# Optimization experiments

Measured on AMD Instinct MI355X. Metric: run time of the kernel, lower is better.

The kernel has to match this reference:

```python
import jax, jax.numpy as jnp
import numpy as np

B, T, V, E, M, L = 1024, 64, 1024, 512, 1024, 32
PE, PO = M // 2, (M - 1) // 2  # even/odd pair counts


def complex_normalize(x, eps=1e-8):
    mag = jnp.sqrt((x.real ** 2 + x.imag ** 2).sum(-1, keepdims=True) + eps)
    return x / mag


def pair_unitary(v0, v1, t, p, r):
    # 2x2 MZI unitary applied to pairs (v0, v1); t/p/r are (P,) broadcast over batch
    c, s = jnp.cos(t), jnp.sin(t)
    eip, eir = jnp.exp(1j * p), jnp.exp(1j * r)
    u11 = eip * c * eir
    u12 = eip * (1j * s)
    u21 = (1j * s) * eir
    u22 = c
    return u11 * v0 + u12 * v1, u21 * v0 + u22 * v1


def setup_inputs() -> dict:
    key = jax.random.key(0)
    ks = jax.random.split(key, 16)
    sE = 1.0 / np.sqrt(E)
    return {
        "context_tokens": jax.random.randint(ks[0], (B, T), 0, V),
        "embed": 0.02 * jax.random.normal(ks[1], (V, E), jnp.float32),
        "W_ih": sE * jax.random.normal(ks[2], (3 * E, E), jnp.float32),
        "W_hh": sE * jax.random.normal(ks[3], (3 * E, E), jnp.float32),
        "b_ih": jnp.zeros((3 * E,), jnp.float32),
        "b_hh": jnp.zeros((3 * E,), jnp.float32),
        "Wc": 0.02 * jax.random.normal(ks[4], (2 * M, E), jnp.float32),
        "bc": jnp.zeros((2 * M,), jnp.float32),
        "phase": 0.1 * jax.random.normal(ks[5], (L, M), jnp.float32),
        "theta_e": 0.1 * jax.random.normal(ks[6], (L, PE), jnp.float32),
        "phi_e": 0.1 * jax.random.normal(ks[7], (L, PE), jnp.float32),
        "rho_e": 0.1 * jax.random.normal(ks[8], (L, PE), jnp.float32),
        "theta_o": 0.1 * jax.random.normal(ks[9], (L, PO), jnp.float32),
        "phi_o": 0.1 * jax.random.normal(ks[10], (L, PO), jnp.float32),
        "rho_o": 0.1 * jax.random.normal(ks[11], (L, PO), jnp.float32),
        "R_real": 0.01 * jax.random.normal(ks[12], (V, M), jnp.float32),
        "R_imag": 0.01 * jax.random.normal(ks[13], (V, M), jnp.float32),
    }


def reference(context_tokens, embed, W_ih, W_hh, b_ih, b_hh, Wc, bc,
              phase, theta_e, phi_e, rho_e, theta_o, phi_o, rho_o,
              R_real, R_imag):
    # --- ContextEncoder: embedding + GRU (torch gate order r,z,n) ---
    x = embed[context_tokens]                      # (B,T,E)
    x_gates = x @ W_ih.T + b_ih                    # (B,T,3E) precomputed input gates

    def gru_step(h, xg):
        ir, iz, in_ = jnp.split(xg, 3, axis=-1)
        hr, hz, hn = jnp.split(h @ W_hh.T + b_hh, 3, axis=-1)
        r = jax.nn.sigmoid(ir + hr)
        z = jax.nn.sigmoid(iz + hz)
        n = jnp.tanh(in_ + r * hn)
        return (1.0 - z) * n + z * h, None

    h0 = jnp.zeros((x.shape[0], embed.shape[1]), x.dtype)
    h, _ = jax.lax.scan(gru_step, h0, jnp.swapaxes(x_gates, 0, 1))  # (B,E)

    zc = h @ Wc.T + bc                              # (B,2M)
    re, im = jnp.split(zc, 2, axis=-1)
    psi = complex_normalize(re + 1j * im)           # (B,M) complex64

    # --- QuantumCore: stack of MZI layers ---
    def layer(psi, p):
        ph, te, pe, re_, to, po, ro = p
        psi = psi * jnp.exp(1j * ph)
        D = psi.shape[1]
        # even pairs (0,1),(2,3),...
        v0, v1 = pair_unitary(psi[:, 0::2], psi[:, 1::2], te, pe, re_)
        psi = psi.at[:, 0::2].set(v0).at[:, 1::2].set(v1)
        # odd pairs (1,2),(3,4),...
        v0, v1 = pair_unitary(psi[:, 1:D - 1:2], psi[:, 2:D:2], to, po, ro)
        psi = psi.at[:, 1:D - 1:2].set(v0).at[:, 2:D:2].set(v1)
        return complex_normalize(psi), None

    psi, _ = jax.lax.scan(layer, psi, (phase, theta_e, phi_e, rho_e,
                                       theta_o, phi_o, rho_o))

    # --- QuantumReadout: Born rule log-probs ---
    R = R_real + 1j * R_imag                        # (V,M)
    amps = psi @ R.T                                # (B,V) complex
    log_mag_sq = jnp.log(amps.real ** 2 + amps.imag ** 2 + 1e-12)
    return log_mag_sq - jax.scipy.special.logsumexp(log_mag_sq, axis=-1, keepdims=True)
```

## Files before the change

### kernel.cpp

```cpp
#include <hip/hip_runtime.h>
#include <math.h>

typedef __bf16 bf16_t;
typedef bf16_t bf16x8 __attribute__((ext_vector_type(8)));
typedef float  f32x4  __attribute__((ext_vector_type(4)));

#define B_  1024
#define T_  64
#define V_  1024
#define E_  512
#define M_  1024
#define L_  32
#define PE_ 512
#define PO_ 511
#define G3_ 1536
#define M2_ 2048

#define MFMA_BF16 __builtin_amdgcn_mfma_f32_16x16x32_bf16

__device__ __forceinline__ void stage16f(float* lds_base, const float* gsrc) {
  __builtin_amdgcn_global_load_lds(
      (const __attribute__((address_space(1))) unsigned int*)gsrc,
      (__attribute__((address_space(3))) unsigned int*)lds_base, 16, 0, 0);
}
__device__ __forceinline__ void stage16b(bf16_t* lds_base, const bf16_t* gsrc) {
  __builtin_amdgcn_global_load_lds(
      (const __attribute__((address_space(1))) unsigned int*)gsrc,
      (__attribute__((address_space(3))) unsigned int*)lds_base, 16, 0, 0);
}

__device__ __forceinline__ size_t tiled_off(int row, int k) {
  return ((size_t)(row >> 4) * 16 + (k >> 5)) * 512 +
         (size_t)(((k >> 3) & 3) * 16 + (row & 15)) * 8 + (k & 7);
}

__device__ __forceinline__ void split_chunk(const float* __restrict__ src,
                                            bf16_t* __restrict__ hi,
                                            bf16_t* __restrict__ lo, int blk,
                                            int tid) {
  int i4 = (blk * 256 + tid) * 4;
  float4 v = *(const float4*)&src[i4];
  float vv[4] = {v.x, v.y, v.z, v.w};
#pragma unroll
  for (int j = 0; j < 4; j++) {
    bf16_t h = (bf16_t)vv[j];
    hi[i4 + j] = h;
    lo[i4 + j] = (bf16_t)(vv[j] - (float)h);
  }
}

__global__ __launch_bounds__(256) void prep_all(
    const float* __restrict__ embed, bf16_t* __restrict__ emb_hi,
    bf16_t* __restrict__ emb_lo, const float* __restrict__ W_ih,
    bf16_t* __restrict__ wih_hi, bf16_t* __restrict__ wih_lo,
    const float* __restrict__ Wc, bf16_t* __restrict__ wc_hi,
    bf16_t* __restrict__ wc_lo, const float* __restrict__ R_real,
    bf16_t* __restrict__ rr_hi, bf16_t* __restrict__ rr_lo,
    const float* __restrict__ R_imag, bf16_t* __restrict__ ri_hi,
    bf16_t* __restrict__ ri_lo, const float* __restrict__ W_hh,
    bf16_t* __restrict__ Wp_hi, bf16_t* __restrict__ Wp_lo,
    const float* __restrict__ phase, const float* __restrict__ th_e,
    const float* __restrict__ ph_e, const float* __restrict__ rh_e,
    float* __restrict__ Uep, const float* __restrict__ th_o,
    const float* __restrict__ ph_o, const float* __restrict__ rh_o,
    float* __restrict__ Uop) {
  const int bid = blockIdx.x, tid = threadIdx.x;
  if (bid < 512) {
    split_chunk(embed, emb_hi, emb_lo, bid, tid);
  } else if (bid < 1280) {
    split_chunk(W_ih, wih_hi, wih_lo, bid - 512, tid);
  } else if (bid < 2304) {
    split_chunk(Wc, wc_hi, wc_lo, bid - 1280, tid);
  } else if (bid < 3328) {
    split_chunk(R_real, rr_hi, rr_lo, bid - 2304, tid);
  } else if (bid < 4352) {
    split_chunk(R_imag, ri_hi, ri_lo, bid - 3328, tid);
  } else if (bid < 5888) {
    int q = bid - 4352;
    int c = q / 96, loc = q % 96;
    int g = loc >> 5, el = loc & 31;
    const float* src = &W_hh[(size_t)(g * 512 + c * 32 + el) * 512];
    if (tid < 64) {
      int k0 = tid * 8;
      float4 v0 = *(const float4*)&src[k0];
      float4 v1 = *(const float4*)&src[k0 + 4];
      float vv[8] = {v0.x, v0.y, v0.z, v0.w, v1.x, v1.y, v1.z, v1.w};
      bf16x8 h8, l8;
#pragma unroll
      for (int j = 0; j < 8; j++) {
        bf16_t h = (bf16_t)vv[j];
        h8[j] = h;
        l8[j] = (bf16_t)(vv[j] - (float)h);
      }
      size_t toff = tiled_off(q, k0);
      *(bf16x8*)&Wp_hi[toff] = h8;
      *(bf16x8*)&Wp_lo[toff] = l8;
    }
  } else if (bid < 5952) {
    int idx = (bid - 5888) * 256 + tid;
    if (idx < L_ * PE_) {
      int l = idx >> 9, p = idx & 511;
      float t = th_e[idx], pp = ph_e[idx], r = rh_e[idx];
      float c = cosf(t), s = sinf(t);
      float cp = cosf(pp), sp = sinf(pp), cr = cosf(r), sr = sinf(r);
      float u11r = c * (cp * cr - sp * sr), u11i = c * (cp * sr + sp * cr);
      float u12r = -s * sp, u12i = s * cp;
      float u21r = -s * sr, u21i = s * cr;
      float u22r = c, u22i = 0.0f;
      float f0 = phase[l * M_ + 2 * p], f1 = phase[l * M_ + 2 * p + 1];
      float c0 = cosf(f0), s0 = sinf(f0), c1 = cosf(f1), s1 = sinf(f1);
      float a, b;
      a = u11r * c0 - u11i * s0; b = u11r * s0 + u11i * c0; u11r = a; u11i = b;
      a = u21r * c0 - u21i * s0; b = u21r * s0 + u21i * c0; u21r = a; u21i = b;
      a = u12r * c1 - u12i * s1; b = u12r * s1 + u12i * c1; u12r = a; u12i = b;
      a = u22r * c1 - u22i * s1; b = u22r * s1 + u22i * c1; u22r = a; u22i = b;
      int j = p & 3, ln = (p >> 2) & 63, hh = p >> 8;
      size_t base = (size_t)l * 4096 + (size_t)(j * 4 + hh) * 256 + ln * 4;
      *(float4*)&Uep[base]       = make_float4(u11r, u11i, u12r, u12i);
      *(float4*)&Uep[base + 512] = make_float4(u21r, u21i, u22r, u22i);
    }
  } else {
    int idx = (bid - 5952) * 256 + tid;
    if (idx < L_ * PO_) {
      int l = idx / PO_, p = idx % PO_;
      float t = th_o[idx], pp = ph_o[idx], r = rh_o[idx];
      float c = cosf(t), s = sinf(t);
      float cp = cosf(pp), sp = sinf(pp), cr = cosf(r), sr = sinf(r);
      int j = p & 3, ln = (p >> 2) & 63, hh = p >> 8;
      size_t base = (size_t)l * 4096 + (size_t)(j * 4 + hh) * 256 + ln * 4;
      *(float4*)&Uop[base] = make_float4(c * (cp * cr - sp * sr),
                                         c * (cp * sr + sp * cr), -s * sp,
                                         s * cp);
      *(float4*)&Uop[base + 512] = make_float4(-s * sr, s * cr, c, 0.0f);
    }
  }
}

__global__ __launch_bounds__(256) void gemm_bt_mfma_split(
    const bf16_t* __restrict__ Ah, const bf16_t* __restrict__ Al,
    const bf16_t* __restrict__ Bh, const bf16_t* __restrict__ Bl,
    float* __restrict__ C, int Ndim, int K) {
  __shared__ bf16_t sAh[64 * 32], sAl[64 * 32], sBh[64 * 32], sBl[64 * 32];
  const int tid = threadIdx.x;
  const int m0 = blockIdx.y * 64, n0 = blockIdx.x * 64;
  const int wave = tid >> 6, lane = tid & 63;
  const int wr = wave >> 1, wc = wave & 1;
  const int quad = lane >> 4, l16 = lane & 15;
  f32x4 acc[2][2] = {};
  const int srow = tid >> 2, sk = (tid & 3) * 8;

  for (int k0 = 0; k0 < K; k0 += 32) {
    bf16x8 ah = *(const bf16x8*)&Ah[(size_t)(m0 + srow) * K + k0 + sk];
    bf16x8 al = *(const bf16x8*)&Al[(size_t)(m0 + srow) * K + k0 + sk];
    bf16x8 bh = *(const bf16x8*)&Bh[(size_t)(n0 + srow) * K + k0 + sk];
    bf16x8 bl = *(const bf16x8*)&Bl[(size_t)(n0 + srow) * K + k0 + sk];
    __syncthreads();
    *(bf16x8*)&sAh[srow * 32 + sk] = ah;
    *(bf16x8*)&sAl[srow * 32 + sk] = al;
    *(bf16x8*)&sBh[srow * 32 + sk] = bh;
    *(bf16x8*)&sBl[srow * 32 + sk] = bl;
    __syncthreads();
    bf16x8 fAh[2], fAl[2], fBh[2], fBl[2];
#pragma unroll
    for (int i = 0; i < 2; i++) {
      fAh[i] = *(const bf16x8*)&sAh[(wr * 32 + i * 16 + l16) * 32 + quad * 8];
      fAl[i] = *(const bf16x8*)&sAl[(wr * 32 + i * 16 + l16) * 32 + quad * 8];
      fBh[i] = *(const bf16x8*)&sBh[(wc * 32 + i * 16 + l16) * 32 + quad * 8];
      fBl[i] = *(const bf16x8*)&sBl[(wc * 32 + i * 16 + l16) * 32 + quad * 8];
    }
#pragma unroll
    for (int i = 0; i < 2; i++)
#pragma unroll
      for (int j = 0; j < 2; j++) {
        acc[i][j] = MFMA_BF16(fAh[i], fBh[j], acc[i][j], 0, 0, 0);
        acc[i][j] = MFMA_BF16(fAh[i], fBl[j], acc[i][j], 0, 0, 0);
        acc[i][j] = MFMA_BF16(fAl[i], fBh[j], acc[i][j], 0, 0, 0);
      }
  }
#pragma unroll
  for (int i = 0; i < 2; i++)
#pragma unroll
    for (int j = 0; j < 2; j++)
#pragma unroll
      for (int r = 0; r < 4; r++) {
        int row = wr * 32 + i * 16 + quad * 4 + r;
        int col = wc * 32 + j * 16 + l16;
        C[(size_t)(m0 + row) * Ndim + n0 + col] = acc[i][j][r];
      }
}

__global__ __launch_bounds__(512) void gru_step11(
    const bf16_t* __restrict__ Hh, const bf16_t* __restrict__ Hl,
    const bf16_t* __restrict__ Wph, const bf16_t* __restrict__ Wpl,
    const int* __restrict__ tok, const float* __restrict__ eg,
    const float* __restrict__ b_ih, const float* __restrict__ b_hh,
    bf16_t* __restrict__ Oh, bf16_t* __restrict__ Ol, int t, int final_) {
  __shared__ bf16_t sB[2][2][24 * 512];
  __shared__ float sC[2][64 * 100];
  __shared__ float sbih[96], sbhh[96];
  const int tid = threadIdx.x;
  const int g = tid >> 8;
  const int gtid = tid & 255;
  const int ct = blockIdx.y, m0 = blockIdx.x * 64;
  const int n0e = ct * 32;
  const int wg = gtid >> 6, lane = tid & 63;
  const int wr = wg >> 1, wc = wg & 1;
  const int quad = lane >> 4, l16 = lane & 15;

#define STAGE_B(buf, it)                                                      \
  {                                                                           \
    _Pragma("unroll") for (int r = 0; r < 6; r++) {                           \
      int c = wg * 6 + r;                                                     \
      int f = (c >= 12) ? (c - 12) : c;                                       \
      int j = f >> 1, ks = f & 1;                                             \
      const bf16_t* srcp = (c < 12) ? Wph : Wpl;                              \
      stage16b(&sB[buf][g][c * 512],                                          \
               &srcp[(size_t)(ct * 6 + j) * 8192 +                            \
                     (size_t)(g * 8 + (it) * 2 + ks) * 512 + lane * 8]);      \
    }                                                                         \
  }

  STAGE_B(0, 0);

  if (tid < 96) {
    sbih[tid] = b_ih[(tid >> 5) * 512 + n0e + (tid & 31)];
    sbhh[tid] = b_hh[(tid >> 5) * 512 + n0e + (tid & 31)];
  }

  float pir[4], piz[4], pin[4], phv[4];
#pragma unroll
  for (int u = 0; u < 4; u++) {
    int flat = u * 512 + tid;
    int row = flat >> 5, el = flat & 31;
    int bb = m0 + row, eG = n0e + el;
    int tk = tok[bb * T_ + t];
    pir[u] = eg[(size_t)tk * G3_ + eG];
    piz[u] = eg[(size_t)tk * G3_ + 512 + eG];
    pin[u] = eg[(size_t)tk * G3_ + 1024 + eG];
    size_t toff = tiled_off(bb, eG);
    phv[u] = (float)Hh[toff] + (float)Hl[toff];
  }

  const size_t aB0 = (size_t)((m0 >> 4) + wr * 2 + 0) * 8192 + (size_t)g * 4096 + lane * 8;
  const size_t aB1 = (size_t)((m0 >> 4) + wr * 2 + 1) * 8192 + (size_t)g * 4096 + lane * 8;

  f32x4 acc[2][3] = {};
  __syncthreads();
#pragma unroll
  for (int it = 0; it < 4; ++it) {
    const int buf = it & 1;
    if (it < 3) STAGE_B(buf ^ 1, it + 1);
    const bf16_t* sBg = &sB[buf][g][0];
#pragma unroll
    for (int ks2 = 0; ks2 < 2; ++ks2) {
      const int kb = it * 2 + ks2;
      const int ko = kb * 512;
      bf16x8 fah[2], fal[2], fbh[3], fbl[3];
      fah[0] = *(const bf16x8*)&Hh[aB0 + ko];
      fah[1] = *(const bf16x8*)&Hh[aB1 + ko];
      fal[0] = *(const bf16x8*)&Hl[aB0 + ko];
      fal[1] = *(const bf16x8*)&Hl[aB1 + ko];
#pragma unroll
      for (int j = 0; j < 3; j++) {
        int f = (wc * 3 + j) * 2 + ks2;
        fbh[j] = *(const bf16x8*)&sBg[f * 512 + lane * 8];
        fbl[j] = *(const bf16x8*)&sBg[(f + 12) * 512 + lane * 8];
      }
#pragma unroll
      for (int i = 0; i < 2; i++)
#pragma unroll
        for (int j = 0; j < 3; j++) {
          acc[i][j] = MFMA_BF16(fah[i], fbh[j], acc[i][j], 0, 0, 0);
          acc[i][j] = MFMA_BF16(fah[i], fbl[j], acc[i][j], 0, 0, 0);
          acc[i][j] = MFMA_BF16(fal[i], fbh[j], acc[i][j], 0, 0, 0);
        }
    }
    __syncthreads();
  }
#undef STAGE_B
#pragma unroll
  for (int i = 0; i < 2; i++)
#pragma unroll
    for (int j = 0; j < 3; j++)
#pragma unroll
      for (int r = 0; r < 4; r++)
        sC[g][(wr * 32 + i * 16 + quad * 4 + r) * 100 + wc * 48 + j * 16 + l16] =
            acc[i][j][r];
  __syncthreads();
#pragma unroll
  for (int u = 0; u < 4; u++) {
    int flat = u * 512 + tid;
    int row = flat >> 5, el = flat & 31;
    int bb = m0 + row, eG = n0e + el;
    float ir = pir[u] + sbih[el];
    float iz = piz[u] + sbih[32 + el];
    float in_ = pin[u] + sbih[64 + el];
    float hr = sC[0][row * 100 + el] + sC[1][row * 100 + el] + sbhh[el];
    float hz = sC[0][row * 100 + 32 + el] + sC[1][row * 100 + 32 + el] + sbhh[32 + el];
    float hn = sC[0][row * 100 + 64 + el] + sC[1][row * 100 + 64 + el] + sbhh[64 + el];
    float r = 1.0f / (1.0f + __expf(-(ir + hr)));
    float z = 1.0f / (1.0f + __expf(-(iz + hz)));
    float targ = fminf(fmaxf(in_ + r * hn, -15.0f), 15.0f);
    float e2 = __expf(2.0f * targ);
    float n = (e2 - 1.0f) / (e2 + 1.0f);
    float hnew = (1.0f - z) * n + z * phv[u];
    bf16_t hh = (bf16_t)hnew;
    bf16_t ll = (bf16_t)(hnew - (float)hh);
    if (final_) {
      size_t hidx = (size_t)bb * 512 + eG;
      Oh[hidx] = hh;
      Ol[hidx] = ll;
    } else {
      size_t toff = tiled_off(bb, eG);
      Oh[toff] = hh;
      Ol[toff] = ll;
    }
  }
}

__device__ inline void apply_u(float4 A, float4 Bv, float& x0r, float& x0i,
                               float& x1r, float& x1i) {
  float n0r = A.x * x0r - A.y * x0i + A.z * x1r - A.w * x1i;
  float n0i = A.x * x0i + A.y * x0r + A.z * x1i + A.w * x1r;
  float n1r = Bv.x * x0r - Bv.y * x0i + Bv.z * x1r - Bv.w * x1i;
  float n1i = Bv.x * x0i + Bv.y * x0r + Bv.z * x1i + Bv.w * x1r;
  x0r = n0r; x0i = n0i; x1r = n1r; x1i = n1i;
}

__global__ __launch_bounds__(256) void qc6(
    const float* __restrict__ zc, const float* __restrict__ bc,
    const float* __restrict__ Uep, const float* __restrict__ Uop,
    bf16_t* __restrict__ prh, bf16_t* __restrict__ prl,
    bf16_t* __restrict__ pih, bf16_t* __restrict__ pil) {
  __shared__ float sU[2][8192];
  __shared__ float sred[4];
  __shared__ float4 sEx[2][2][2];
  const int tid = threadIdx.x;
  const int wave = tid >> 6, lane = tid & 63;
  const int wb = wave >> 1, h = wave & 1;
  const int b = blockIdx.x * 2 + wb;
  const int e0 = h * 512 + lane * 8;

#define STAGE_L(l, buf)                                                       \
  {                                                                           \
    _Pragma("unroll") for (int r = 0; r < 8; r++) {                           \
      int c = wave * 8 + r;                                                   \
      const float* src = (c < 16)                                             \
          ? &Uep[(size_t)(l) * 4096 + c * 256 + lane * 4]                     \
          : &Uop[(size_t)(l) * 4096 + (c - 16) * 256 + lane * 4];             \
      stage16f(&sU[buf][c * 256], src);                                       \
    }                                                                         \
  }

  float xr[8], xi[8];
  {
    const float4* zr4 = (const float4*)&zc[(size_t)b * M2_ + e0];
    const float4* zi4 = (const float4*)&zc[(size_t)b * M2_ + M_ + e0];
    const float4* br4 = (const float4*)&bc[e0];
    const float4* bi4 = (const float4*)&bc[M_ + e0];
#pragma unroll
    for (int q = 0; q < 2; q++) {
      float4 a = zr4[q], bb = br4[q];
      xr[4 * q + 0] = a.x + bb.x; xr[4 * q + 1] = a.y + bb.y;
      xr[4 * q + 2] = a.z + bb.z; xr[4 * q + 3] = a.w + bb.w;
      float4 c2 = zi4[q], d = bi4[q];
      xi[4 * q + 0] = c2.x + d.x; xi[4 * q + 1] = c2.y + d.y;
      xi[4 * q + 2] = c2.z + d.z; xi[4 * q + 3] = c2.w + d.w;
    }
  }
  STAGE_L(0, 0);
  {
    float s = 0.0f;
#pragma unroll
    for (int k = 0; k < 8; k++) s += xr[k] * xr[k] + xi[k] * xi[k];
    for (int off = 32; off; off >>= 1) s += __shfl_xor(s, off);
    if (lane == 0) sred[wave] = s;
    __syncthreads();
    float inv = 1.0f / sqrtf(sred[2 * wb] + sred[2 * wb + 1] + 1e-8f);
#pragma unroll
    for (int k = 0; k < 8; k++) { xr[k] *= inv; xi[k] *= inv; }
  }
  if (h == 0 && lane == 63) sEx[0][wb][0] = make_float4(xr[6], xi[6], xr[7], xi[7]);
  if (h == 1 && lane == 0)  sEx[0][wb][1] = make_float4(xr[0], xi[0], xr[1], xi[1]);
  __syncthreads();

#pragma unroll 1
  for (int l = 0; l < L_; ++l) {
    const int buf = l & 1;
    if (l + 1 < L_) STAGE_L(l + 1, 1 - buf);
    const float* Ub = &sU[buf][0];
    const float* Ob = &sU[buf][4096];
    float4 par = make_float4(0.f, 0.f, 0.f, 0.f);
    if (h == 0 && lane == 63) par = sEx[buf][wb][1];
    if (h == 1 && lane == 0)  par = sEx[buf][wb][0];
#pragma unroll
    for (int j = 0; j < 4; j++) {
      float4 A  = *(const float4*)&Ub[(j * 4 + h) * 256 + lane * 4];
      float4 Bv = *(const float4*)&Ub[(j * 4 + 2 + h) * 256 + lane * 4];
      apply_u(A, Bv, xr[2 * j], xi[2 * j], xr[2 * j + 1], xi[2 * j + 1]);
    }
    float exr = 0.f, exi = 0.f;
    if (h == 0 && lane == 63) {
      float4 Ae = *(const float4*)&Ub[1 * 256];
      exr = Ae.x * par.x - Ae.y * par.y + Ae.z * par.z - Ae.w * par.w;
      exi = Ae.x * par.y + Ae.y * par.x + Ae.z * par.w + Ae.w * par.z;
    }
    if (h == 1 && lane == 0) {
      float4 Be = *(const float4*)&Ub[14 * 256 + 252];
      exr = Be.x * par.x - Be.y * par.y + Be.z * par.z - Be.w * par.w;
      exi = Be.x * par.y + Be.y * par.x + Be.z * par.w + Be.w * par.z;
    }
#pragma unroll
    for (int j = 0; j < 3; j++) {
      float4 A  = *(const float4*)&Ob[(j * 4 + h) * 256 + lane * 4];
      float4 Bv = *(const float4*)&Ob[(j * 4 + 2 + h) * 256 + lane * 4];
      apply_u(A, Bv, xr[2 * j + 1], xi[2 * j + 1], xr[2 * j + 2], xi[2 * j + 2]);
    }
    float nr = __shfl_down(xr[0], 1), ni = __shfl_down(xi[0], 1);
    if (h == 0 && lane == 63) { nr = exr; ni = exi; }
    float srr = 0.f, sii = 0.f;
    if (!(h == 1 && lane == 63)) {
      float4 A3 = *(const float4*)&Ob[(12 + h) * 256 + lane * 4];
      float4 B3 = *(const float4*)&Ob[(14 + h) * 256 + lane * 4];
      float n0r = A3.x * xr[7] - A3.y * xi[7] + A3.z * nr - A3.w * ni;
      float n0i = A3.x * xi[7] + A3.y * xr[7] + A3.z * ni + A3.w * nr;
      srr = B3.x * xr[7] - B3.y * xi[7] + B3.z * nr - B3.w * ni;
      sii = B3.x * xi[7] + B3.y * xr[7] + B3.z * ni + B3.w * nr;
      xr[7] = n0r; xi[7] = n0i;
    }
    float nx0r = 0.f, nx0i = 0.f;
    if (h == 1 && lane == 0) {
      float4 Bc = *(const float4*)&Ob[14 * 256 + 252];
      nx0r = Bc.x * exr - Bc.y * exi + Bc.z * xr[0] - Bc.w * xi[0];
      nx0i = Bc.x * exi + Bc.y * exr + Bc.z * xi[0] + Bc.w * xr[0];
    }
    float rr = __shfl_up(srr, 1), ri2 = __shfl_up(sii, 1);
    if (lane > 0) { xr[0] = rr; xi[0] = ri2; }
    if (h == 1 && lane == 0) { xr[0] = nx0r; xi[0] = nx0i; }
    if (h == 0 && lane == 63)
      sEx[1 - buf][wb][0] = make_float4(xr[6], xi[6], xr[7], xi[7]);
    if (h == 1 && lane == 0)
      sEx[1 - buf][wb][1] = make_float4(xr[0], xi[0], xr[1], xi[1]);
    __syncthreads();
  }
#undef STAGE_L
  size_t base = (size_t)b * M_ + e0;
  bf16x8 vh, vl, wh, wl;
#pragma unroll
  for (int k = 0; k < 8; k++) {
    float vr = xr[k], vi = xi[k];
    bf16_t h1 = (bf16_t)vr;
    vh[k] = h1; vl[k] = (bf16_t)(vr - (float)h1);
    bf16_t h2 = (bf16_t)vi;
    wh[k] = h2; wl[k] = (bf16_t)(vi - (float)h2);
  }
  *(bf16x8*)&prh[base] = vh;
  *(bf16x8*)&prl[base] = vl;
  *(bf16x8*)&pih[base] = wh;
  *(bf16x8*)&pil[base] = wl;
}

__global__ __launch_bounds__(256) void readout_mfma(
    const bf16_t* __restrict__ Arh, const bf16_t* __restrict__ Arl,
    const bf16_t* __restrict__ Aih, const bf16_t* __restrict__ Ail,
    const bf16_t* __restrict__ Brh, const bf16_t* __restrict__ Brl,
    const bf16_t* __restrict__ Bih, const bf16_t* __restrict__ Bil,
    float* __restrict__ out) {
  __shared__ bf16_t sArh[64 * 32], sArl[64 * 32], sAih[64 * 32], sAil[64 * 32];
  __shared__ bf16_t sBrh[64 * 32], sBrl[64 * 32], sBih[64 * 32], sBil[64 * 32];
  const int tid = threadIdx.x;
  const int b0 = blockIdx.y * 64, v0 = blockIdx.x * 64;
  const int wave = tid >> 6, lane = tid & 63;
  const int wr = wave >> 1, wc = wave & 1;
  const int quad = lane >> 4, l16 = lane & 15;
  f32x4 aP[2][2] = {}, aQ[2][2] = {}, aI[2][2] = {};
  const int srow = tid >> 2, sk = (tid & 3) * 8;

  for (int k0 = 0; k0 < M_; k0 += 32) {
    size_t aoff = (size_t)(b0 + srow) * M_ + k0 + sk;
    size_t boff = (size_t)(v0 + srow) * M_ + k0 + sk;
    bf16x8 v0r = *(const bf16x8*)&Arh[aoff];
    bf16x8 v1r = *(const bf16x8*)&Arl[aoff];
    bf16x8 v2r = *(const bf16x8*)&Aih[aoff];
    bf16x8 v3r = *(const bf16x8*)&Ail[aoff];
    bf16x8 v4r = *(const bf16x8*)&Brh[boff];
    bf16x8 v5r = *(const bf16x8*)&Brl[boff];
    bf16x8 v6r = *(const bf16x8*)&Bih[boff];
    bf16x8 v7r = *(const bf16x8*)&Bil[boff];
    __syncthreads();
    *(bf16x8*)&sArh[srow * 32 + sk] = v0r;
    *(bf16x8*)&sArl[srow * 32 + sk] = v1r;
    *(bf16x8*)&sAih[srow * 32 + sk] = v2r;
    *(bf16x8*)&sAil[srow * 32 + sk] = v3r;
    *(bf16x8*)&sBrh[srow * 32 + sk] = v4r;
    *(bf16x8*)&sBrl[srow * 32 + sk] = v5r;
    *(bf16x8*)&sBih[srow * 32 + sk] = v6r;
    *(bf16x8*)&sBil[srow * 32 + sk] = v7r;
    __syncthreads();
    bf16x8 fArh[2], fArl[2], fAih[2], fAil[2], fBrh[2], fBrl[2], fBih[2], fBil[2];
#pragma unroll
    for (int i = 0; i < 2; i++) {
      int ra = (wr * 32 + i * 16 + l16) * 32 + quad * 8;
      int rb = (wc * 32 + i * 16 + l16) * 32 + quad * 8;
      fArh[i] = *(const bf16x8*)&sArh[ra];
      fArl[i] = *(const bf16x8*)&sArl[ra];
      fAih[i] = *(const bf16x8*)&sAih[ra];
      fAil[i] = *(const bf16x8*)&sAil[ra];
      fBrh[i] = *(const bf16x8*)&sBrh[rb];
      fBrl[i] = *(const bf16x8*)&sBrl[rb];
      fBih[i] = *(const bf16x8*)&sBih[rb];
      fBil[i] = *(const bf16x8*)&sBil[rb];
    }
#pragma unroll
    for (int i = 0; i < 2; i++)
#pragma unroll
      for (int j = 0; j < 2; j++) {
        aP[i][j] = MFMA_BF16(fArh[i], fBrh[j], aP[i][j], 0, 0, 0);
        aP[i][j] = MFMA_BF16(fArh[i], fBrl[j], aP[i][j], 0, 0, 0);
        aP[i][j] = MFMA_BF16(fArl[i], fBrh[j], aP[i][j], 0, 0, 0);
        aQ[i][j] = MFMA_BF16(fAih[i], fBih[j], aQ[i][j], 0, 0, 0);
        aQ[i][j] = MFMA_BF16(fAih[i], fBil[j], aQ[i][j], 0, 0, 0);
        aQ[i][j] = MFMA_BF16(fAil[i], fBih[j], aQ[i][j], 0, 0, 0);
        aI[i][j] = MFMA_BF16(fArh[i], fBih[j], aI[i][j], 0, 0, 0);
        aI[i][j] = MFMA_BF16(fArh[i], fBil[j], aI[i][j], 0, 0, 0);
        aI[i][j] = MFMA_BF16(fArl[i], fBih[j], aI[i][j], 0, 0, 0);
        aI[i][j] = MFMA_BF16(fAih[i], fBrh[j], aI[i][j], 0, 0, 0);
        aI[i][j] = MFMA_BF16(fAih[i], fBrl[j], aI[i][j], 0, 0, 0);
        aI[i][j] = MFMA_BF16(fAil[i], fBrh[j], aI[i][j], 0, 0, 0);
      }
  }
#pragma unroll
  for (int i = 0; i < 2; i++)
#pragma unroll
    for (int j = 0; j < 2; j++)
#pragma unroll
      for (int r = 0; r < 4; r++) {
        int row = wr * 32 + i * 16 + quad * 4 + r;
        int col = wc * 32 + j * 16 + l16;
        float re = aP[i][j][r] - aQ[i][j][r];
        float im = aI[i][j][r];
        out[(size_t)(b0 + row) * V_ + v0 + col] = logf(re * re + im * im + 1e-12f);
      }
}

__global__ __launch_bounds__(256) void lse_kernel(float* __restrict__ out) {
  __shared__ float redm[4], reds[4];
  const int b = blockIdx.x, t = threadIdx.x;
  float4 v = *(float4*)&out[(size_t)b * V_ + 4 * t];
  float mx = fmaxf(fmaxf(v.x, v.y), fmaxf(v.z, v.w));
  for (int off = 32; off; off >>= 1) mx = fmaxf(mx, __shfl_down(mx, off, 64));
  if ((t & 63) == 0) redm[t >> 6] = mx;
  __syncthreads();
  mx = fmaxf(fmaxf(redm[0], redm[1]), fmaxf(redm[2], redm[3]));
  float s = expf(v.x - mx) + expf(v.y - mx) + expf(v.z - mx) + expf(v.w - mx);
  for (int off = 32; off; off >>= 1) s += __shfl_down(s, off, 64);
  if ((t & 63) == 0) reds[t >> 6] = s;
  __syncthreads();
  s = reds[0] + reds[1] + reds[2] + reds[3];
  float lse = mx + logf(s);
  v.x -= lse; v.y -= lse; v.z -= lse; v.w -= lse;
  *(float4*)&out[(size_t)b * V_ + 4 * t] = v;
}

extern "C" void kernel_launch(void* const* d_in, const int* in_sizes, int n_in,
                              void* d_out, int out_size, void* d_ws, size_t ws_size,
                              hipStream_t stream) {
  const int*   tokens = (const int*)d_in[0];
  const float* embed  = (const float*)d_in[1];
  const float* W_ih   = (const float*)d_in[2];
  const float* W_hh   = (const float*)d_in[3];
  const float* b_ih   = (const float*)d_in[4];
  const float* b_hh   = (const float*)d_in[5];
  const float* Wc     = (const float*)d_in[6];
  const float* bc     = (const float*)d_in[7];
  const float* phase  = (const float*)d_in[8];
  const float* theta_e = (const float*)d_in[9];
  const float* phi_e  = (const float*)d_in[10];
  const float* rho_e  = (const float*)d_in[11];
  const float* theta_o = (const float*)d_in[12];
  const float* phi_o  = (const float*)d_in[13];
  const float* rho_o  = (const float*)d_in[14];
  const float* R_real = (const float*)d_in[15];
  const float* R_imag = (const float*)d_in[16];
  float* out = (float*)d_out;

  char* w = (char*)d_ws;
  auto alloc = [&](size_t bytes) -> void* {
    void* p = (void*)w;
    w += (bytes + 255) & ~(size_t)255;
    return p;
  };
  char* region0 = w;
  bf16_t* emb_hi = (bf16_t*)alloc((size_t)V_ * E_ * 2);
  bf16_t* emb_lo = (bf16_t*)alloc((size_t)V_ * E_ * 2);
  bf16_t* wih_hi = (bf16_t*)alloc((size_t)G3_ * E_ * 2);
  bf16_t* wih_lo = (bf16_t*)alloc((size_t)G3_ * E_ * 2);
  bf16_t* wc_hi  = (bf16_t*)alloc((size_t)M2_ * E_ * 2);
  bf16_t* wc_lo  = (bf16_t*)alloc((size_t)M2_ * E_ * 2);
  char* region1 = w;
  float*  eg     = (float*)alloc((size_t)V_ * G3_ * 4);
  bf16_t* Wp_hi  = (bf16_t*)alloc((size_t)G3_ * E_ * 2);
  bf16_t* Wp_lo  = (bf16_t*)alloc((size_t)G3_ * E_ * 2);
  bf16_t* h0_hi = (bf16_t*)alloc((size_t)B_ * E_ * 2);
  bf16_t* h0_lo = (bf16_t*)alloc((size_t)B_ * E_ * 2);
  bf16_t* h1_hi = (bf16_t*)alloc((size_t)B_ * E_ * 2);
  bf16_t* h1_lo = (bf16_t*)alloc((size_t)B_ * E_ * 2);
  bf16_t* rr_hi = (bf16_t*)alloc((size_t)V_ * M_ * 2);
  bf16_t* rr_lo = (bf16_t*)alloc((size_t)V_ * M_ * 2);
  bf16_t* ri_hi = (bf16_t*)alloc((size_t)V_ * M_ * 2);
  bf16_t* ri_lo = (bf16_t*)alloc((size_t)V_ * M_ * 2);
  float*  Uep   = (float*)alloc((size_t)L_ * 4096 * 4);
  float*  Uop   = (float*)alloc((size_t)L_ * 4096 * 4);

  float*  zc  = (float*)region1;
  bf16_t* prh = (bf16_t*)(region0 + 0 * 2097152);
  bf16_t* prl = (bf16_t*)(region0 + 1 * 2097152);
  bf16_t* pih = (bf16_t*)(region0 + 2 * 2097152);
  bf16_t* pil = (bf16_t*)(region0 + 3 * 2097152);

  hipMemsetAsync(h0_hi, 0, (size_t)B_ * E_ * 2 * 2, stream);

  prep_all<<<6016, 256, 0, stream>>>(
      embed, emb_hi, emb_lo, W_ih, wih_hi, wih_lo, Wc, wc_hi, wc_lo, R_real,
      rr_hi, rr_lo, R_imag, ri_hi, ri_lo, W_hh, Wp_hi, Wp_lo, phase, theta_e,
      phi_e, rho_e, Uep, theta_o, phi_o, rho_o, Uop);

  {
    dim3 grid(G3_ / 64, V_ / 64);
    gemm_bt_mfma_split<<<grid, 256, 0, stream>>>(emb_hi, emb_lo, wih_hi, wih_lo,
                                                 eg, G3_, E_);
  }

  for (int t = 0; t < T_; ++t) {
    const bf16_t* ih = (t & 1) ? h1_hi : h0_hi;
    const bf16_t* il = (t & 1) ? h1_lo : h0_lo;
    bf16_t* oh = (t & 1) ? h0_hi : h1_hi;
    bf16_t* ol = (t & 1) ? h0_lo : h1_lo;
    dim3 grid(16, 16);
    gru_step11<<<grid, 512, 0, stream>>>(ih, il, Wp_hi, Wp_lo, tokens, eg,
                                         b_ih, b_hh, oh, ol, t,
                                         (t == T_ - 1) ? 1 : 0);
  }

  {
    dim3 grid(M2_ / 64, B_ / 64);
    gemm_bt_mfma_split<<<grid, 256, 0, stream>>>(h0_hi, h0_lo, wc_hi, wc_lo,
                                                 zc, M2_, E_);
  }

  qc6<<<B_ / 2, 256, 0, stream>>>(zc, bc, Uep, Uop, prh, prl, pih, pil);

  {
    dim3 grid(V_ / 64, B_ / 64);
    readout_mfma<<<grid, 256, 0, stream>>>(prh, prl, pih, pil, rr_hi, rr_lo,
                                           ri_hi, ri_lo, out);
  }

  lse_kernel<<<B_, 256, 0, stream>>>(out);
}
```

Before: 862.5 us.

## Split readout GEMM K dimension across two thread groups with LDS reduction

The readout kernel now runs 512 threads per block as two 256-thread groups. Each group handles half of the K=1024 reduction with its own LDS tiles, and the two partial results are summed through shared memory before the log-magnitude is written. The aim is more waves per tile and more latency hiding, since the grid is only 256 blocks. In exchange it uses much more LDS per block (a 32 KB reduction buffer plus doubled staging), adds a block-wide sync, and the syncs inside the loop now span both groups.

```diff
diff --git a/kernel.cpp b/kernel.cpp
--- a/kernel.cpp
+++ b/kernel.cpp
@@ -460,25 +460,29 @@
   *(bf16x8*)&pil[base] = wl;
 }
 
-__global__ __launch_bounds__(256) void readout_mfma(
+__global__ __launch_bounds__(512) void readout_ks(
     const bf16_t* __restrict__ Arh, const bf16_t* __restrict__ Arl,
     const bf16_t* __restrict__ Aih, const bf16_t* __restrict__ Ail,
     const bf16_t* __restrict__ Brh, const bf16_t* __restrict__ Brl,
     const bf16_t* __restrict__ Bih, const bf16_t* __restrict__ Bil,
     float* __restrict__ out) {
-  __shared__ bf16_t sArh[64 * 32], sArl[64 * 32], sAih[64 * 32], sAil[64 * 32];
-  __shared__ bf16_t sBrh[64 * 32], sBrl[64 * 32], sBih[64 * 32], sBil[64 * 32];
+  __shared__ bf16_t sArh[2][64 * 32], sArl[2][64 * 32], sAih[2][64 * 32], sAil[2][64 * 32];
+  __shared__ bf16_t sBrh[2][64 * 32], sBrl[2][64 * 32], sBih[2][64 * 32], sBil[2][64 * 32];
+  __shared__ float sRe[2][64 * 64];
+  __shared__ float sIm[2][64 * 64];
   const int tid = threadIdx.x;
+  const int g = tid >> 8, gtid = tid & 255;
   const int b0 = blockIdx.y * 64, v0 = blockIdx.x * 64;
-  const int wave = tid >> 6, lane = tid & 63;
+  const int wave = gtid >> 6, lane = tid & 63;
   const int wr = wave >> 1, wc = wave & 1;
   const int quad = lane >> 4, l16 = lane & 15;
   f32x4 aP[2][2] = {}, aQ[2][2] = {}, aI[2][2] = {};
-  const int srow = tid >> 2, sk = (tid & 3) * 8;
-
-  for (int k0 = 0; k0 < M_; k0 += 32) {
-    size_t aoff = (size_t)(b0 + srow) * M_ + k0 + sk;
-    size_t boff = (size_t)(v0 + srow) * M_ + k0 + sk;
+  const int srow = gtid >> 2, sk = (gtid & 3) * 8;
+  const int kb = g * 512;
+
+  for (int k0 = 0; k0 < 512; k0 += 32) {
+    size_t aoff = (size_t)(b0 + srow) * M_ + kb + k0 + sk;
+    size_t boff = (size_t)(v0 + srow) * M_ + kb + k0 + sk;
     bf16x8 v0r = *(const bf16x8*)&Arh[aoff];
     bf16x8 v1r = *(const bf16x8*)&Arl[aoff];
     bf16x8 v2r = *(const bf16x8*)&Aih[aoff];
@@ -488,28 +492,28 @@
     bf16x8 v6r = *(const bf16x8*)&Bih[boff];
     bf16x8 v7r = *(const bf16x8*)&Bil[boff];
     __syncthreads();
-    *(bf16x8*)&sArh[srow * 32 + sk] = v0r;
-    *(bf16x8*)&sArl[srow * 32 + sk] = v1r;
-    *(bf16x8*)&sAih[srow * 32 + sk] = v2r;
-    *(bf16x8*)&sAil[srow * 32 + sk] = v3r;
-    *(bf16x8*)&sBrh[srow * 32 + sk] = v4r;
-    *(bf16x8*)&sBrl[srow * 32 + sk] = v5r;
-    *(bf16x8*)&sBih[srow * 32 + sk] = v6r;
-    *(bf16x8*)&sBil[srow * 32 + sk] = v7r;
+    *(bf16x8*)&sArh[g][srow * 32 + sk] = v0r;
+    *(bf16x8*)&sArl[g][srow * 32 + sk] = v1r;
+    *(bf16x8*)&sAih[g][srow * 32 + sk] = v2r;
+    *(bf16x8*)&sAil[g][srow * 32 + sk] = v3r;
+    *(bf16x8*)&sBrh[g][srow * 32 + sk] = v4r;
+    *(bf16x8*)&sBrl[g][srow * 32 + sk] = v5r;
+    *(bf16x8*)&sBih[g][srow * 32 + sk] = v6r;
+    *(bf16x8*)&sBil[g][srow * 32 + sk] = v7r;
     __syncthreads();
     bf16x8 fArh[2], fArl[2], fAih[2], fAil[2], fBrh[2], fBrl[2], fBih[2], fBil[2];
 #pragma unroll
     for (int i = 0; i < 2; i++) {
       int ra = (wr * 32 + i * 16 + l16) * 32 + quad * 8;
       int rb = (wc * 32 + i * 16 + l16) * 32 + quad * 8;
-      fArh[i] = *(const bf16x8*)&sArh[ra];
-      fArl[i] = *(const bf16x8*)&sArl[ra];
-      fAih[i] = *(const bf16x8*)&sAih[ra];
-      fAil[i] = *(const bf16x8*)&sAil[ra];
-      fBrh[i] = *(const bf16x8*)&sBrh[rb];
-      fBrl[i] = *(const bf16x8*)&sBrl[rb];
-      fBih[i] = *(const bf16x8*)&sBih[rb];
-      fBil[i] = *(const bf16x8*)&sBil[rb];
+      fArh[i] = *(const bf16x8*)&sArh[g][ra];
+      fArl[i] = *(const bf16x8*)&sArl[g][ra];
+      fAih[i] = *(const bf16x8*)&sAih[g][ra];
+      fAil[i] = *(const bf16x8*)&sAil[g][ra];
+      fBrh[i] = *(const bf16x8*)&sBrh[g][rb];
+      fBrl[i] = *(const bf16x8*)&sBrl[g][rb];
+      fBih[i] = *(const bf16x8*)&sBih[g][rb];
+      fBil[i] = *(const bf16x8*)&sBil[g][rb];
     }
 #pragma unroll
     for (int i = 0; i < 2; i++)
@@ -537,10 +541,18 @@
       for (int r = 0; r < 4; r++) {
         int row = wr * 32 + i * 16 + quad * 4 + r;
         int col = wc * 32 + j * 16 + l16;
-        float re = aP[i][j][r] - aQ[i][j][r];
-        float im = aI[i][j][r];
-        out[(size_t)(b0 + row) * V_ + v0 + col] = logf(re * re + im * im + 1e-12f);
+        sRe[g][row * 64 + col] = aP[i][j][r] - aQ[i][j][r];
+        sIm[g][row * 64 + col] = aI[i][j][r];
       }
+  __syncthreads();
+#pragma unroll
+  for (int u = 0; u < 8; u++) {
+    int idx = u * 512 + tid;
+    float re = sRe[0][idx] + sRe[1][idx];
+    float im = sIm[0][idx] + sIm[1][idx];
+    int row = idx >> 6, col = idx & 63;
+    out[(size_t)(b0 + row) * V_ + v0 + col] = logf(re * re + im * im + 1e-12f);
+  }
 }
 
 __global__ __launch_bounds__(256) void lse_kernel(float* __restrict__ out) {
@@ -652,8 +664,8 @@
 
   {
     dim3 grid(V_ / 64, B_ / 64);
-    readout_mfma<<<grid, 256, 0, stream>>>(prh, prl, pih, pil, rr_hi, rr_lo,
-                                           ri_hi, ri_lo, out);
+    readout_ks<<<grid, 512, 0, stream>>>(prh, prl, pih, pil, rr_hi, rr_lo,
+                                         ri_hi, ri_lo, out);
   }
 
   lse_kernel<<<B_, 256, 0, stream>>>(out);
```

Result: no change. 870.9 us (+1.0%).
